# Optimization experiments

Measured on AMD Instinct MI355X. Metric: run time of the kernel, lower is better.

Reference implementation:

```python
import jax, jax.numpy as jnp
import numpy as np

NUM_LEVELS = 4
RADIUS = 4


def setup_inputs() -> dict:
    key = jax.random.key(0)
    k1, k2, k3 = jax.random.split(key, 3)
    B, C, H, W = 2, 256, 64, 64
    N = 4
    fmap1 = jax.random.normal(k1, (B, C, H, W), dtype=jnp.float32)
    fmap2 = jax.random.normal(k2, (B, C, H, W), dtype=jnp.float32)
    # coords channel 0 = x in [0, W-1], channel 1 = y in [0, H-1]
    coords = jax.random.uniform(k3, (B, N, 2, H, W), dtype=jnp.float32) * (W - 1)
    return {"fmap1": fmap1, "fmap2": fmap2, "coords": coords}


def _bilinear_gather(corr, x, y):
    """Zero-padded bilinear sampling (grid_sample align_corners=True semantics).
    corr: (B, P, h2, w2) per-query-pixel correlation maps.
    x, y: (B, N, P, K2) absolute pixel coords into (w2, h2).
    Returns (B, N, P, K2)."""
    Bv, P, h2, w2 = corr.shape
    x0 = jnp.floor(x)
    y0 = jnp.floor(y)
    wx1 = x - x0
    wy1 = y - y0
    b = jnp.arange(Bv)[:, None, None, None]
    p = jnp.arange(P)[None, None, :, None]

    def corner(yi, xi):
        valid = (xi >= 0) & (xi <= w2 - 1) & (yi >= 0) & (yi <= h2 - 1)
        xi_c = jnp.clip(xi, 0, w2 - 1).astype(jnp.int32)
        yi_c = jnp.clip(yi, 0, h2 - 1).astype(jnp.int32)
        v = corr[b, p, yi_c, xi_c]
        return jnp.where(valid, v, jnp.zeros((), corr.dtype))

    v00 = corner(y0, x0)
    v01 = corner(y0, x0 + 1)
    v10 = corner(y0 + 1, x0)
    v11 = corner(y0 + 1, x0 + 1)
    return ((1 - wy1) * (1 - wx1) * v00 + (1 - wy1) * wx1 * v01
            + wy1 * (1 - wx1) * v10 + wy1 * wx1 * v11)


def reference(fmap1, fmap2, coords):
    B, C, H, W = fmap1.shape
    _, N = coords.shape[0], coords.shape[1]
    P = H * W
    r = RADIUS
    K = 2 * r + 1
    K2 = K * K

    # All-pairs correlation: (B, P_query, H2, W2), scaled by 1/sqrt(C) (RAFT)
    f1 = fmap1.reshape(B, C, P)
    f2 = fmap2.reshape(B, C, P)
    corr = jnp.einsum('bcp,bcq->bpq', f1, f2) / jnp.sqrt(jnp.asarray(C, fmap1.dtype))
    corr = corr.reshape(B, P, H, W)

    # Pyramid via 2x2 average pooling (stride 2, no padding)
    pyramid = [corr]
    c = corr
    for _ in range(NUM_LEVELS - 1):
        h2, w2 = c.shape[-2:]
        c = c.reshape(B, P, h2 // 2, 2, w2 // 2, 2).mean(axis=(3, 5))
        pyramid.append(c)

    # Window offsets. Faithful to the torch code: delta = stack(meshgrid(dy, dx, 'ij'))
    # so delta[...,0] = yy is added to the x-channel, delta[...,1] = xx to the y-channel.
    d = jnp.linspace(-r, r, K).astype(coords.dtype)
    yy, xx = jnp.meshgrid(d, d, indexing='ij')
    off_x = yy.reshape(1, 1, 1, K2)  # added to coords[...,0]
    off_y = xx.reshape(1, 1, 1, K2)  # added to coords[...,1]

    cx = coords[:, :, 0].reshape(B, N, P)  # (B, N, P)
    cy = coords[:, :, 1].reshape(B, N, P)

    outs = []
    for i, cl in enumerate(pyramid):
        scale = jnp.asarray(2.0 ** i, coords.dtype)
        x = cx[..., None] / scale + off_x  # (B, N, P, K2)
        y = cy[..., None] / scale + off_y
        v = _bilinear_gather(cl, x, y)     # (B, N, P, K2)
        outs.append(v.reshape(B, N, H, W, K2))

    out = jnp.concatenate(outs, axis=-1)   # (B, N, H, W, L*K2)
    Ctot = out.shape[-1]
    # Matches torch: contiguous (B,N,H,W,C) reshaped row-major to (B, N*C, H, W)
    out = out.reshape(B, N * Ctot, H, W)
    return out.astype(jnp.float32)
```

## Files before the change

### kernel.cpp

```cpp
#include <hip/hip_runtime.h>
#include <hip/hip_bf16.h>
#include <cstdint>

#define B_    2
#define C_    256
#define H_    64
#define W_    64
#define P_    (H_*W_)
#define N_    4
#define RAD   4
#define K2_   81
#define CTOT  (4*K2_)

typedef __bf16 bf16x8 __attribute__((ext_vector_type(8)));
typedef float  f32x4  __attribute__((ext_vector_type(4)));

__device__ __forceinline__ void gload_lds16(const void* g, void* l) {
    __builtin_amdgcn_global_load_lds(
        (const __attribute__((address_space(1))) void*)g,
        (__attribute__((address_space(3))) void*)l,
        16, 0, 0);
}

__global__ void transpose_cvt(const float* __restrict__ in0,
                              const float* __restrict__ in1,
                              __hip_bfloat16* __restrict__ out0,
                              __hip_bfloat16* __restrict__ out1) {
    __shared__ float tile[32][33];
    const int z     = blockIdx.z;
    const int which = z >> 1;
    const int b     = z & 1;
    const float* in          = which ? in1  : in0;
    __hip_bfloat16* out      = which ? out1 : out0;
    const int p0 = blockIdx.x * 32;
    const int c0 = blockIdx.y * 32;
    const int tx = threadIdx.x;
    const int ty = threadIdx.y;
    const float* src = in + ((size_t)b * C_ + c0) * P_ + p0;
    #pragma unroll
    for (int i = 0; i < 32; i += 8)
        tile[ty + i][tx] = src[(size_t)(ty + i) * P_ + tx];
    __syncthreads();
    __hip_bfloat16* dst = out + ((size_t)b * P_ + p0) * C_ + c0;
    #pragma unroll
    for (int i = 0; i < 32; i += 8)
        dst[(size_t)(ty + i) * C_ + tx] = __float2bfloat16(tile[tx][ty + i]);
}

#define TSTR 136

__global__ __launch_bounds__(256) void gemm_corr(
    const short* __restrict__ f1t,
    const short* __restrict__ f2t,
    __hip_bfloat16* __restrict__ corr0,
    __hip_bfloat16* __restrict__ corr1)
{
    __shared__ short smem[128 * TSTR];
    short* As = smem;
    short* Bs = smem + 8192;

    const int tid  = threadIdx.x;
    const int lane = tid & 63;
    const int wv   = tid >> 6;
    const int wm   = (wv >> 1) * 64;
    const int wn   = (wv & 1) * 64;
    const int b    = blockIdx.z;
    const int bx   = blockIdx.x;
    const int m0   = blockIdx.y * 128;
    const int n0   = bx * 128;
    const int qd   = lane >> 4;
    const int l15  = lane & 15;

    const short* gA[4];
    const short* gB[4];
    int ldsOff[4];
    #pragma unroll
    for (int it = 0; it < 4; ++it) {
        const int ci = it * 256 + tid;
        const int r  = ci >> 3;
        const int cp = ci & 7;
        const int kc = cp ^ (r & 7);
        gA[it] = f1t + ((size_t)(b * P_ + m0 + r)) * C_ + kc * 8;
        gB[it] = f2t + ((size_t)(b * P_ + n0 + r)) * C_ + kc * 8;
        ldsOff[it] = (it * 256 + wv * 64) * 8;
    }

    int aAddr[4][2], bAddr[4][2];
    #pragma unroll
    for (int i = 0; i < 4; ++i) {
        const int m = wm + i * 16 + l15;
        const int n = wn + i * 16 + l15;
        #pragma unroll
        for (int s = 0; s < 2; ++s) {
            const int lc = s * 4 + qd;
            aAddr[i][s] = m * 64 + ((lc ^ (m & 7)) * 8);
            bAddr[i][s] = n * 64 + ((lc ^ (n & 7)) * 8);
        }
    }

    f32x4 zero = {0.f, 0.f, 0.f, 0.f};
    f32x4 acc[4][4];
    #pragma unroll
    for (int mi = 0; mi < 4; ++mi)
        #pragma unroll
        for (int ni = 0; ni < 4; ++ni)
            acc[mi][ni] = zero;

    for (int kt = 0; kt < 4; ++kt) {
        const int k0 = kt * 64;
        #pragma unroll
        for (int it = 0; it < 4; ++it) {
            gload_lds16(gA[it] + k0, As + ldsOff[it]);
            gload_lds16(gB[it] + k0, Bs + ldsOff[it]);
        }
        __syncthreads();
        #pragma unroll
        for (int s = 0; s < 2; ++s) {
            bf16x8 af[4], bfr[4];
            #pragma unroll
            for (int i = 0; i < 4; ++i) {
                af[i]  = *(const bf16x8*)(As + aAddr[i][s]);
                bfr[i] = *(const bf16x8*)(Bs + bAddr[i][s]);
            }
            #pragma unroll
            for (int mi = 0; mi < 4; ++mi)
                #pragma unroll
                for (int ni = 0; ni < 4; ++ni)
                    acc[mi][ni] = __builtin_amdgcn_mfma_f32_16x16x32_bf16(
                        af[mi], bfr[ni], acc[mi][ni], 0, 0, 0);
        }
        __syncthreads();
    }

    const float sc = 0.0625f;
    __hip_bfloat16* tile = (__hip_bfloat16*)smem;
    #pragma unroll
    for (int mi = 0; mi < 4; ++mi) {
        #pragma unroll
        for (int ni = 0; ni < 4; ++ni) {
            #pragma unroll
            for (int r = 0; r < 4; ++r) {
                const int rl = wm + mi * 16 + qd * 4 + r;
                const int cl = wn + ni * 16 + l15;
                tile[rl * TSTR + cl] = __float2bfloat16(acc[mi][ni][r] * sc);
            }
        }
    }
    __syncthreads();

    #pragma unroll
    for (int i = 0; i < 8; ++i) {
        const int cid = i * 256 + tid;
        const int tr  = cid >> 4;
        const int tc  = cid & 15;
        const float4 v = *(const float4*)(smem + tr * TSTR + tc * 8);
        *(float4*)(corr0 + ((size_t)(b * P_ + m0 + tr)) * P_ + n0 + tc * 8) = v;
    }

    #pragma unroll
    for (int i = 0; i < 8; ++i) {
        const int oid = i * 256 + tid;
        const int pr  = oid >> 4;
        const int j   = oid & 15;
        const uint32_t* r0 = (const uint32_t*)(smem + pr * TSTR + 4 * j);
        const uint32_t* r1 = (const uint32_t*)(smem + pr * TSTR + 64 + 4 * j);
        const uint32_t a01 = r0[0], a23 = r0[1];
        const uint32_t b01 = r1[0], b23 = r1[1];
        const float v0 = (__uint_as_float(a01 << 16) +
                          __uint_as_float(a01 & 0xffff0000u) +
                          __uint_as_float(b01 << 16) +
                          __uint_as_float(b01 & 0xffff0000u)) * 0.25f;
        const float v1 = (__uint_as_float(a23 << 16) +
                          __uint_as_float(a23 & 0xffff0000u) +
                          __uint_as_float(b23 << 16) +
                          __uint_as_float(b23 & 0xffff0000u)) * 0.25f;
        union { __hip_bfloat16 h[2]; uint32_t u; } pk;
        pk.h[0] = __float2bfloat16(v0);
        pk.h[1] = __float2bfloat16(v1);
        *(uint32_t*)(corr1 + ((size_t)(b * P_ + m0 + pr)) * 1024 +
                     bx * 32 + 2 * j) = pk.u;
    }
}

__global__ __launch_bounds__(256) void gather5(
    const float* __restrict__ coords,
    const __hip_bfloat16* __restrict__ c0,
    const __hip_bfloat16* __restrict__ c1,
    float* __restrict__ out) {
    __shared__ float pool_sm[320];
    __shared__ float patch[4][440];

    const int tid  = threadIdx.x;
    const int lane = tid & 63;
    const int n    = tid >> 6;
    const int bp   = blockIdx.x;
    const int b    = bp >> 12;
    const int p    = bp & (P_ - 1);

    const __hip_bfloat16* c0b = c0 + (size_t)bp * 4096;
    const __hip_bfloat16* c1b = c1 + (size_t)bp * 1024;

    const float cx = coords[((size_t)((b * N_ + n) * 2 + 0)) * P_ + p];
    const float cy = coords[((size_t)((b * N_ + n) * 2 + 1)) * P_ + p];
    int x0i[4], y0i[4];
    float w00[4], w01[4], w10[4], w11[4];
    #pragma unroll
    for (int l = 0; l < 4; ++l) {
        const float inv = (l == 0) ? 1.f : (l == 1) ? 0.5f : (l == 2) ? 0.25f : 0.125f;
        const float x = cx * inv, y = cy * inv;
        const float x0f = floorf(x), y0f = floorf(y);
        const float wx = x - x0f, wy = y - y0f;
        x0i[l] = (int)x0f - RAD;
        y0i[l] = (int)y0f - RAD;
        w00[l] = (1.f - wy) * (1.f - wx);
        w01[l] = (1.f - wy) * wx;
        w10[l] = wy * (1.f - wx);
        w11[l] = wy * wx;
    }

    float pv[2][2];
    #pragma unroll
    for (int lvl = 0; lvl < 2; ++lvl) {
        const __hip_bfloat16* src = lvl ? c1b : c0b;
        const int hw = lvl ? 32 : 64;
        const int sh = lvl ? 5 : 6;
        #pragma unroll
        for (int it = 0; it < 2; ++it) {
            const int idx = it * 64 + lane;
            const int r   = idx / 11;
            const int cc  = idx - r * 11;
            const int gr  = y0i[lvl] + r, gc = x0i[lvl] + cc;
            float v = 0.f;
            if ((idx < 110) & (cc < 10) & ((unsigned)gr < (unsigned)hw) &
                ((unsigned)gc < (unsigned)hw))
                v = __bfloat162float(src[(gr << sh) + gc]);
            pv[lvl][it] = v;
        }
    }

    {
        const int y2 = tid >> 4, x2 = tid & 15;
        const uint32_t u0 = *(const uint32_t*)(c1b + (2 * y2) * 32 + 2 * x2);
        const uint32_t u1 = *(const uint32_t*)(c1b + (2 * y2 + 1) * 32 + 2 * x2);
        const float a0 = __uint_as_float(u0 << 16);
        const float a1 = __uint_as_float(u0 & 0xffff0000u);
        const float b0 = __uint_as_float(u1 << 16);
        const float b1 = __uint_as_float(u1 & 0xffff0000u);
        pool_sm[tid] = (a0 + a1 + b0 + b1) * 0.25f;
    }
    __syncthreads();
    if (tid < 64) {
        const int y3 = tid >> 3, x3 = tid & 7;
        const float* r0 = pool_sm + (2 * y3) * 16 + 2 * x3;
        pool_sm[256 + tid] = (r0[0] + r0[1] + r0[16] + r0[17]) * 0.25f;
    }
    __syncthreads();

    float* pw = patch[n];
    #pragma unroll
    for (int lvl = 0; lvl < 2; ++lvl) {
        #pragma unroll
        for (int it = 0; it < 2; ++it) {
            const int idx = it * 64 + lane;
            if (idx < 110) pw[lvl * 110 + idx] = pv[lvl][it];
        }
    }
    #pragma unroll
    for (int lvl = 2; lvl < 4; ++lvl) {
        const int hw   = (lvl == 2) ? 16 : 8;
        const int sh   = (lvl == 2) ? 4 : 3;
        const int base = (lvl == 2) ? 0 : 256;
        #pragma unroll
        for (int it = 0; it < 2; ++it) {
            const int idx = it * 64 + lane;
            if (idx < 110) {
                const int r  = idx / 11;
                const int cc = idx - r * 11;
                const int gr = y0i[lvl] + r, gc = x0i[lvl] + cc;
                float v = 0.f;
                if ((cc < 10) & ((unsigned)gr < (unsigned)hw) &
                    ((unsigned)gc < (unsigned)hw))
                    v = pool_sm[base + (gr << sh) + gc];
                pw[lvl * 110 + idx] = v;
            }
        }
    }

    const size_t obase = ((size_t)(b * N_ + n) * P_ + p) * CTOT;
    #pragma unroll
    for (int lvl = 0; lvl < 4; ++lvl) {
        const float* pl = pw + lvl * 110;
        float* ol = out + obase + lvl * K2_;
        #pragma unroll
        for (int it = 0; it < 2; ++it) {
            const int k2 = it * 64 + lane;
            if (k2 < K2_) {
                const int ki = k2 / 9;
                const int kj = k2 - ki * 9;
                const float* pr = pl + kj * 11 + ki;
                ol[k2] = w00[lvl] * pr[0] + w01[lvl] * pr[1] +
                         w10[lvl] * pr[11] + w11[lvl] * pr[12];
            }
        }
    }
}

extern "C" void kernel_launch(void* const* d_in, const int* in_sizes, int n_in,
                              void* d_out, int out_size, void* d_ws, size_t ws_size,
                              hipStream_t stream) {
    const float* fmap1  = (const float*)d_in[0];
    const float* fmap2  = (const float*)d_in[1];
    const float* coords = (const float*)d_in[2];
    float* out = (float*)d_out;

    char* ws = (char*)d_ws;
    __hip_bfloat16* f1t = (__hip_bfloat16*)ws;
    __hip_bfloat16* f2t = (__hip_bfloat16*)(ws + 4194304);
    __hip_bfloat16* c0  = (__hip_bfloat16*)(ws + 8388608);
    __hip_bfloat16* c1  = (__hip_bfloat16*)(ws + 75497472);

    {
        dim3 grid(P_ / 32, C_ / 32, 2 * B_);
        dim3 blk(32, 8);
        transpose_cvt<<<grid, blk, 0, stream>>>(fmap1, fmap2, f1t, f2t);
    }

    {
        dim3 grid(P_ / 128, P_ / 128, B_);
        gemm_corr<<<grid, 256, 0, stream>>>((const short*)f1t, (const short*)f2t,
                                            c0, c1);
    }

    gather5<<<B_ * P_, 256, 0, stream>>>(coords, c0, c1, out);
}
```

Baseline: 126.9 us.

## Load GEMM MFMA fragments directly from global memory, dropping LDS staging

The correlation GEMM no longer stages A/B tiles in shared memory through global_load_lds with swizzled layouts and barriers. Each lane now reads its bf16x8 fragments straight from global memory, and the K loop is fully unrolled over eight 32-wide segments. This removes LDS traffic and the syncthreads between K tiles. In exchange, each wave re-reads data that other waves share, so global/L2 traffic rises, and loads become strided per lane (16 rows × 16B), which may hurt coalescing.

```diff
diff --git a/kernel.cpp b/kernel.cpp
--- a/kernel.cpp
+++ b/kernel.cpp
@@ -14,13 +14,6 @@
 
 typedef __bf16 bf16x8 __attribute__((ext_vector_type(8)));
 typedef float  f32x4  __attribute__((ext_vector_type(4)));
-
-__device__ __forceinline__ void gload_lds16(const void* g, void* l) {
-    __builtin_amdgcn_global_load_lds(
-        (const __attribute__((address_space(1))) void*)g,
-        (__attribute__((address_space(3))) void*)l,
-        16, 0, 0);
-}
 
 __global__ void transpose_cvt(const float* __restrict__ in0,
                               const float* __restrict__ in1,
@@ -56,8 +49,6 @@
     __hip_bfloat16* __restrict__ corr1)
 {
     __shared__ short smem[128 * TSTR];
-    short* As = smem;
-    short* Bs = smem + 8192;
 
     const int tid  = threadIdx.x;
     const int lane = tid & 63;
@@ -71,31 +62,12 @@
     const int qd   = lane >> 4;
     const int l15  = lane & 15;
 
-    const short* gA[4];
-    const short* gB[4];
-    int ldsOff[4];
-    #pragma unroll
-    for (int it = 0; it < 4; ++it) {
-        const int ci = it * 256 + tid;
-        const int r  = ci >> 3;
-        const int cp = ci & 7;
-        const int kc = cp ^ (r & 7);
-        gA[it] = f1t + ((size_t)(b * P_ + m0 + r)) * C_ + kc * 8;
-        gB[it] = f2t + ((size_t)(b * P_ + n0 + r)) * C_ + kc * 8;
-        ldsOff[it] = (it * 256 + wv * 64) * 8;
-    }
-
-    int aAddr[4][2], bAddr[4][2];
+    const short* aB[4];
+    const short* bB[4];
     #pragma unroll
     for (int i = 0; i < 4; ++i) {
-        const int m = wm + i * 16 + l15;
-        const int n = wn + i * 16 + l15;
-        #pragma unroll
-        for (int s = 0; s < 2; ++s) {
-            const int lc = s * 4 + qd;
-            aAddr[i][s] = m * 64 + ((lc ^ (m & 7)) * 8);
-            bAddr[i][s] = n * 64 + ((lc ^ (n & 7)) * 8);
-        }
+        aB[i] = f1t + ((size_t)(b * P_ + m0 + wm + i * 16 + l15)) * C_ + qd * 8;
+        bB[i] = f2t + ((size_t)(b * P_ + n0 + wn + i * 16 + l15)) * C_ + qd * 8;
     }
 
     f32x4 zero = {0.f, 0.f, 0.f, 0.f};
@@ -106,30 +78,21 @@
         for (int ni = 0; ni < 4; ++ni)
             acc[mi][ni] = zero;
 
-    for (int kt = 0; kt < 4; ++kt) {
-        const int k0 = kt * 64;
-        #pragma unroll
-        for (int it = 0; it < 4; ++it) {
-            gload_lds16(gA[it] + k0, As + ldsOff[it]);
-            gload_lds16(gB[it] + k0, Bs + ldsOff[it]);
-        }
-        __syncthreads();
-        #pragma unroll
-        for (int s = 0; s < 2; ++s) {
-            bf16x8 af[4], bfr[4];
+    #pragma unroll
+    for (int seg = 0; seg < 8; ++seg) {
+        const int ko = seg * 32;
+        bf16x8 af[4], bfr[4];
+        #pragma unroll
+        for (int i = 0; i < 4; ++i) {
+            af[i]  = *(const bf16x8*)(aB[i] + ko);
+            bfr[i] = *(const bf16x8*)(bB[i] + ko);
+        }
+        #pragma unroll
+        for (int mi = 0; mi < 4; ++mi)
             #pragma unroll
-            for (int i = 0; i < 4; ++i) {
-                af[i]  = *(const bf16x8*)(As + aAddr[i][s]);
-                bfr[i] = *(const bf16x8*)(Bs + bAddr[i][s]);
-            }
-            #pragma unroll
-            for (int mi = 0; mi < 4; ++mi)
-                #pragma unroll
-                for (int ni = 0; ni < 4; ++ni)
-                    acc[mi][ni] = __builtin_amdgcn_mfma_f32_16x16x32_bf16(
-                        af[mi], bfr[ni], acc[mi][ni], 0, 0, 0);
-        }
-        __syncthreads();
+            for (int ni = 0; ni < 4; ++ni)
+                acc[mi][ni] = __builtin_amdgcn_mfma_f32_16x16x32_bf16(
+                    af[mi], bfr[ni], acc[mi][ni], 0, 0, 0);
     }
 
     const float sc = 0.0625f;
```

Result: slower. 160.0 us (+26.1%).
